# Performance work log

Hardware: AMD Instinct MI355X
Metric: run time of the kernel (lower is better)

The kernel has to match this reference:

```python
import jax, jax.numpy as jnp
import numpy as np

B, T, DIM, DZ = 512, 256, 128, 256
H = 2 * DZ  # LSTM hidden size (per direction)
RESIDUAL = False


def _lstm_cell(xt, h, c, Wih, Whh, bih, bhh):
    # PyTorch gate order: input, forget, cell, output
    g = xt @ Wih.T + bih + h @ Whh.T + bhh
    i, f, gg, o = jnp.split(g, 4, axis=-1)
    c2 = jax.nn.sigmoid(f) * c + jax.nn.sigmoid(i) * jnp.tanh(gg)
    h2 = jax.nn.sigmoid(o) * jnp.tanh(c2)
    return h2, c2


def _masked_lstm(xs, lengths, Wih, Whh, bih, bhh):
    # Packed-sequence semantics: state frozen and output zero past each length.
    Bn, Tn, _ = xs.shape
    Hn = Whh.shape[1]

    def step(carry, inp):
        h, c = carry
        xt, t = inp
        h2, c2 = _lstm_cell(xt, h, c, Wih, Whh, bih, bhh)
        m = (t < lengths)[:, None]
        h = jnp.where(m, h2, h)
        c = jnp.where(m, c2, c)
        return (h, c), jnp.where(m, h2, 0.0)

    init = (jnp.zeros((Bn, Hn), xs.dtype), jnp.zeros((Bn, Hn), xs.dtype))
    _, hs = jax.lax.scan(step, init, (xs.swapaxes(0, 1), jnp.arange(Tn)))
    return hs.swapaxes(0, 1)  # [B,T,H]


def setup_inputs() -> dict:
    key = jax.random.key(0)
    ks = jax.random.split(key, 24)
    rn = lambda k, *s: jax.random.normal(k, s, jnp.float32) * 0.02
    z = jnp.zeros
    return {
        "x": jax.random.normal(ks[0], (B, T, DIM), jnp.float32),
        "x_lengths": jax.random.randint(ks[1], (B,), 1, T + 1),
        "norm_g": jnp.ones((T, DIM)), "norm_b": z((T, DIM)),
        "We": rn(ks[2], DZ, DIM), "be": z((DZ,)),
        "Wih_f": rn(ks[3], 4 * H, DZ), "Whh_f": rn(ks[4], 4 * H, H),
        "bih_f": z((4 * H,)), "bhh_f": z((4 * H,)),
        "Wih_b": rn(ks[5], 4 * H, DZ), "Whh_b": rn(ks[6], 4 * H, H),
        "bih_b": z((4 * H,)), "bhh_b": z((4 * H,)),
        "W1e": rn(ks[7], H, 2 * H), "b1e": z((H,)),
        "W2e": rn(ks[8], DZ, H), "b2e": z((DZ,)),
        "Wd": rn(ks[9], DZ, DZ), "bd": z((DZ,)),
        "Wp1": rn(ks[10], DZ, DZ), "bp1": z((DZ,)),
        "Wp2": rn(ks[11], DIM, DZ), "bp2": z((DIM,)),
        "Wih_d": rn(ks[12], 4 * H, DZ + DIM), "Whh_d": rn(ks[13], 4 * H, H),
        "bih_d": z((4 * H,)), "bhh_d": z((4 * H,)),
        "W1d": rn(ks[14], DZ, H), "b1d": z((DZ,)),
        "W2d": rn(ks[15], DIM, DZ), "b2d": z((DIM,)),
    }


def _forward(x, x_lengths, norm_g, norm_b, We, be,
             Wih_f, Whh_f, bih_f, bhh_f, Wih_b, Whh_b, bih_b, bhh_b,
             W1e, b1e, W2e, b2e,
             Wd, bd, Wp1, bp1, Wp2, bp2,
             Wih_d, Whh_d, bih_d, bhh_d, W1d, b1d, W2d, b2d):
    # ----- encoder -----
    # LayerNorm over the last two dims [T, DIM] per sample
    mu = x.mean(axis=(1, 2), keepdims=True)
    var = x.var(axis=(1, 2), keepdims=True)
    xn = (x - mu) / jnp.sqrt(var + 1e-5) * norm_g + norm_b
    xe = jax.nn.relu(xn @ We.T + be)  # [B,T,DZ]

    hs_f = _masked_lstm(xe, x_lengths, Wih_f, Whh_f, bih_f, bhh_f)
    # backward direction: reverse each valid prefix, run, scatter back
    rev_idx = jnp.clip(x_lengths[:, None] - 1 - jnp.arange(T)[None, :], 0)  # [B,T]
    xe_rev = jnp.take_along_axis(xe, rev_idx[:, :, None], axis=1)
    hs_b_rev = _masked_lstm(xe_rev, x_lengths, Wih_b, Whh_b, bih_b, bhh_b)
    hs_b = jnp.take_along_axis(hs_b_rev, rev_idx[:, :, None], axis=1)
    valid = (jnp.arange(T)[None, :] < x_lengths[:, None])[:, :, None]
    out = jnp.concatenate([hs_f, jnp.where(valid, hs_b, 0.0)], axis=-1)  # [B,T,2H]
    out = out.sum(axis=1) / x_lengths[:, None].astype(x.dtype)
    out = jax.nn.relu(out @ W1e.T + b1e)
    zlat = out @ W2e.T + b2e  # [B,DZ]

    x0 = jax.nn.relu(zlat @ Wd.T + bd)
    pose0 = jax.nn.relu(x0 @ Wp1.T + bp1) @ Wp2.T + bp2  # [B,DIM]
    h0 = jnp.zeros((x.shape[0], H), x.dtype)

    def dstep(carry, _):
        h, c, pose = carry
        inp = jnp.concatenate([x0, pose], axis=1)
        h2, c2 = _lstm_cell(inp, h, c, Wih_d, Whh_d, bih_d, bhh_d)
        h_ = jax.nn.relu(h2 @ W1d.T + b1d)
        new_pose = h_ @ W2d.T + b2d
        if RESIDUAL:
            new_pose = new_pose + pose
        return (h2, c2, new_pose), new_pose

    _, poses = jax.lax.scan(dstep, (h0, h0, pose0), None, length=T)
    return poses.swapaxes(0, 1)  # [B,T,DIM]


def reference(x, x_lengths, norm_g, norm_b, We, be,
              Wih_f, Whh_f, bih_f, bhh_f, Wih_b, Whh_b, bih_b, bhh_b,
              W1e, b1e, W2e, b2e,
              Wd, bd, Wp1, bp1, Wp2, bp2,
              Wih_d, Whh_d, bih_d, bhh_d, W1d, b1d, W2d, b2d):
    dec = _forward(x, x_lengths, norm_g, norm_b, We, be,
                   Wih_f, Whh_f, bih_f, bhh_f, Wih_b, Whh_b, bih_b, bhh_b,
                   W1e, b1e, W2e, b2e,
                   Wd, bd, Wp1, bp1, Wp2, bp2,
                   Wih_d, Whh_d, bih_d, bhh_d, W1d, b1d, W2d, b2d)
    return (x, dec, x_lengths)
```

## Files before the change

kernel.cpp:

```cpp
#include <hip/hip_runtime.h>
#include <stdint.h>
#include <math.h>

typedef unsigned short u16;
typedef unsigned char u8;
typedef unsigned u32;
typedef unsigned long long u64;
typedef short s16x8 __attribute__((ext_vector_type(8)));
typedef int i32x2 __attribute__((ext_vector_type(2)));
typedef __bf16 bv8 __attribute__((ext_vector_type(8)));
typedef float f32x4 __attribute__((ext_vector_type(4)));

#define DEV static __device__ __forceinline__

DEV float b2f(u16 x){ union{unsigned u; float f;} v; v.u=((unsigned)x)<<16; return v.f; }
DEV u16 f2b(float f){ union{float f; unsigned u;} v; v.f=f; unsigned u=v.u; u += 0x7fff + ((u>>16)&1u); return (u16)(u>>16); }
DEV float sigm(float x){ return 1.f/(1.f+__expf(-x)); }
DEV float tanh_(float x){ float cx=fminf(fmaxf(x,-20.f),20.f); float e=__expf(2.f*cx); return (e-1.f)/(e+1.f); }
DEV f32x4 mfma16(bv8 a, bv8 b, f32x4 c){ return __builtin_amdgcn_mfma_f32_16x16x32_bf16(a,b,c,0,0,0); }
DEV f32x4 mfma8(u64 a, u64 b, f32x4 c){ return __builtin_amdgcn_mfma_f32_16x16x32_fp8_fp8((long)a,(long)b,c,0,0,0); }
DEV bv8 ldf(const u16* p){ return __builtin_bit_cast(bv8, *(const s16x8*)p); }
DEV bv8 cvt(const s16x8& v){ return __builtin_bit_cast(bv8, v); }
DEV u8 f2e4(float f){ return (u8)__builtin_amdgcn_cvt_pk_fp8_f32(f, f, 0, false); }

DEV unsigned ald4(const unsigned* p){ return __hip_atomic_load(p, __ATOMIC_RELAXED, __HIP_MEMORY_SCOPE_AGENT); }

DEV void gld16(s16x8& d, const u16* p){
  asm volatile("global_load_dwordx4 %0, %1, off sc0 sc1" : "=&v"(d) : "v"(p));
}
DEV void gld8(u64& d, const u8* p){
  asm volatile("global_load_dwordx2 %0, %1, off sc0 sc1" : "=&v"(d) : "v"(p));
}
DEV void gldc8(u64& d, const u8* p){
  asm volatile("global_load_dwordx2 %0, %1, off" : "=&v"(d) : "v"(p));
}
DEV void gst8(u16* p, u64 v){
  asm volatile("global_store_dwordx2 %0, %1, off sc0 sc1" :: "v"(p), "v"(v) : "memory");
}
DEV void gst4(u8* p, u32 v){
  asm volatile("global_store_dword %0, %1, off sc0 sc1" :: "v"(p), "v"(v) : "memory");
}
template<int N> DEV void wvm(){
  asm volatile("s_waitcnt vmcnt(%0)" :: "i"(N) : "memory");
  __builtin_amdgcn_sched_barrier(0);
}

DEV void arrive(unsigned* flags, int my, unsigned e){
  asm volatile("s_waitcnt vmcnt(0)" ::: "memory");
  __syncthreads();
  if (threadIdx.x==0)
    __hip_atomic_store(&flags[my*32], e, __ATOMIC_RELAXED, __HIP_MEMORY_SCOPE_AGENT);
}
DEV void waitflags(unsigned* flags, int lo, int n, unsigned e){
  int t = (int)threadIdx.x;
  if (t>=lo && t<lo+n){
    unsigned v;
    do {
      asm volatile("global_load_dword %0, %1, off sc0 sc1\ns_waitcnt vmcnt(0)" : "=&v"(v) : "v"(flags + t*32) : "memory");
      if (v>=e) break;
      __builtin_amdgcn_s_sleep(1);
    } while (1);
  }
  __syncthreads();
}

struct CvtJobs { const float* s[14]; u16* d[14]; int start[14]; };

__global__ __launch_bounds__(256) void cvt_w(CvtJobs J){
  int blk = blockIdx.x, tid = threadIdx.x;
  int j = 0;
  #pragma unroll
  for (int k=1;k<14;k++) if (blk >= J.start[k]) j = k;
  size_t idx = (size_t)(blk - J.start[j])*2048 + (size_t)tid*8;
  const f32x4* ps = (const f32x4*)(J.s[j] + idx);
  f32x4 a = ps[0], b = ps[1];
  s16x8 o;
  #pragma unroll
  for (int i=0;i<4;i++){ o[i]=(short)f2b(a[i]); o[4+i]=(short)f2b(b[i]); }
  *(s16x8*)(J.d[j] + idx) = o;
}

struct Cvt8Jobs { const float* s[4]; u8* d[4]; int start[4]; };

__global__ __launch_bounds__(256) void cvt_w8(Cvt8Jobs J){
  int blk = blockIdx.x, tid = threadIdx.x;
  int j = 0;
  #pragma unroll
  for (int k=1;k<4;k++) if (blk >= J.start[k]) j = k;
  size_t idx = (size_t)(blk - J.start[j])*2048 + (size_t)tid*8;
  const f32x4* ps = (const f32x4*)(J.s[j] + idx);
  f32x4 a = ps[0], b = ps[1];
  int w0 = __builtin_amdgcn_cvt_pk_fp8_f32(a[0]*64.f, a[1]*64.f, 0, false);
  w0 = __builtin_amdgcn_cvt_pk_fp8_f32(a[2]*64.f, a[3]*64.f, w0, true);
  int w1 = __builtin_amdgcn_cvt_pk_fp8_f32(b[0]*64.f, b[1]*64.f, 0, false);
  w1 = __builtin_amdgcn_cvt_pk_fp8_f32(b[2]*64.f, b[3]*64.f, w1, true);
  i32x2 o; o[0]=w0; o[1]=w1;
  *(i32x2*)(J.d[j] + idx) = o;
}

__global__ __launch_bounds__(256) void tr_w2d(const u16* __restrict__ in, u16* __restrict__ out){
  int idx = blockIdx.x*256 + threadIdx.x;
  int r = idx>>7, p = idx&127;
  out[idx] = in[p*256 + r];
}

__global__ __launch_bounds__(256) void pb_k(const float* __restrict__ Wihd, const float* __restrict__ b2d,
                                            float* __restrict__ pb){
  int g = blockIdx.x*256 + threadIdx.x;
  const float* row = Wihd + (size_t)g*384 + 256;
  float s = 0.f;
  for (int p=0;p<128;p++) s += row[p]*b2d[p];
  pb[g] = s;
}

__global__ __launch_bounds__(256) void ln_stats(const float* __restrict__ x,
                                                float* __restrict__ mu, float* __restrict__ rstd){
  int b = blockIdx.x;
  const float* xb = x + (size_t)b*32768;
  float s1=0.f, s2=0.f;
  for (int i = threadIdx.x*4; i < 32768; i += 256*4){
    f32x4 v = *(const f32x4*)(xb+i);
    #pragma unroll
    for (int j=0;j<4;j++){ float f = v[j]; s1+=f; s2+=f*f; }
  }
  #pragma unroll
  for (int o=32;o>0;o>>=1){ s1 += __shfl_down(s1,o); s2 += __shfl_down(s2,o); }
  __shared__ float r1[4], r2[4];
  int w = threadIdx.x>>6;
  if ((threadIdx.x&63)==0){ r1[w]=s1; r2[w]=s2; }
  __syncthreads();
  if (threadIdx.x==0){
    float a=0.f,c=0.f;
    for (int i=0;i<4;i++){ a+=r1[i]; c+=r2[i]; }
    float m=a/32768.f, v=c/32768.f-m*m;
    mu[b]=m; rstd[b]=1.f/sqrtf(v+1e-5f);
  }
}

__global__ __launch_bounds__(256) void ln_gemm(const float* __restrict__ x,
    const float* __restrict__ mu, const float* __restrict__ rstd,
    const float* __restrict__ g, const float* __restrict__ bn,
    const u16* __restrict__ Wb, const float* __restrict__ be, u8* __restrict__ xe){
  __shared__ __align__(16) u16 As[128*32];
  __shared__ __align__(16) u16 Ws[128*32];
  int tid=threadIdx.x, lane=tid&63, wid=tid>>6;
  int wr=wid>>1, wc=wid&1;
  long m0=(long)blockIdx.y*128, n0=(long)blockIdx.x*128;
  int lr=lane&15, lk=(lane>>4)*8;
  f32x4 acc[4][4];
  #pragma unroll
  for (int i=0;i<4;i++)
    #pragma unroll
    for (int j=0;j<4;j++) acc[i][j]=(f32x4){0.f,0.f,0.f,0.f};

  for (int k0=0;k0<128;k0+=32){
    __syncthreads();
    #pragma unroll
    for (int c=tid;c<512;c+=256){
      int row=c>>2, kb=(c&3)*8;
      long R=m0+row;
      int b=(int)(R>>8), tt=(int)(R&255);
      float m=mu[b], rs=rstd[b];
      const f32x4* px=(const f32x4*)(x + R*128 + k0+kb);
      const f32x4* pg=(const f32x4*)(g + tt*128 + k0+kb);
      const f32x4* pb=(const f32x4*)(bn + tt*128 + k0+kb);
      f32x4 x0=px[0], x1=px[1], g0=pg[0], g1=pg[1], b0=pb[0], b1=pb[1];
      s16x8 o;
      #pragma unroll
      for (int j=0;j<4;j++){
        o[j]   = (short)f2b((x0[j]-m)*rs*g0[j] + b0[j]);
        o[4+j] = (short)f2b((x1[j]-m)*rs*g1[j] + b1[j]);
      }
      *(s16x8*)(As + row*32 + kb) = o;
    }
    #pragma unroll
    for (int c=tid;c<512;c+=256){
      int row=c>>2, kb=(c&3)*8;
      *(s16x8*)(Ws + row*32 + kb) = *(const s16x8*)(Wb + (n0+row)*128 + k0+kb);
    }
    __syncthreads();
    bv8 af[4], bf[4];
    #pragma unroll
    for (int i=0;i<4;i++) af[i] = ldf(As + (wr*64+i*16+lr)*32 + lk);
    #pragma unroll
    for (int j=0;j<4;j++) bf[j] = ldf(Ws + (wc*64+j*16+lr)*32 + lk);
    #pragma unroll
    for (int i=0;i<4;i++)
      #pragma unroll
      for (int j=0;j<4;j++) acc[i][j] = mfma16(af[i], bf[j], acc[i][j]);
  }
  #pragma unroll
  for (int i=0;i<4;i++)
    #pragma unroll
    for (int j=0;j<4;j++)
      #pragma unroll
      for (int r=0;r<4;r++){
        int m = wr*64+i*16+(lane>>4)*4+r;
        int n = wc*64+j*16+lr;
        float v = acc[i][j][r] + be[n0+n];
        xe[(m0+m)*256 + n0+n] = f2e4(fmaxf(v,0.f)*16.f);
      }
}

template<int BM, int BN, bool RELU, bool OUTF32>
__global__ __launch_bounds__(256) void gemm_bt(const u16* __restrict__ A, int lda,
                                               const u16* __restrict__ W, int ldw,
                                               const float* __restrict__ bias1, const float* __restrict__ bias2,
                                               u16* __restrict__ Cb, float* __restrict__ Cf, int ldc, int K){
  constexpr int BK=32;
  constexpr int FM=BM/32, FN=BN/32;
  __shared__ __align__(16) u16 As[BM*BK];
  __shared__ __align__(16) u16 Ws[BN*BK];
  int tid=threadIdx.x, lane=tid&63, wid=tid>>6;
  int wr=wid>>1, wc=wid&1;
  long m0=(long)blockIdx.y*BM, n0=(long)blockIdx.x*BN;
  int lr=lane&15, lk=(lane>>4)*8;
  f32x4 acc[FM][FN];
  #pragma unroll
  for (int i=0;i<FM;i++)
    #pragma unroll
    for (int j=0;j<FN;j++) acc[i][j] = (f32x4){0.f,0.f,0.f,0.f};
  for (int k0=0;k0<K;k0+=BK){
    __syncthreads();
    #pragma unroll
    for (int c=tid;c<BM*4;c+=256){
      int row=c>>2, kb=(c&3)*8;
      *(s16x8*)(As + row*BK + kb) = *(const s16x8*)(A + (m0+row)*lda + k0+kb);
    }
    #pragma unroll
    for (int c=tid;c<BN*4;c+=256){
      int row=c>>2, kb=(c&3)*8;
      *(s16x8*)(Ws + row*BK + kb) = *(const s16x8*)(W + (n0+row)*ldw + k0+kb);
    }
    __syncthreads();
    bv8 af[FM], bf[FN];
    #pragma unroll
    for (int i=0;i<FM;i++) af[i] = ldf(As + (wr*(BM/2)+i*16+lr)*BK + lk);
    #pragma unroll
    for (int j=0;j<FN;j++) bf[j] = ldf(Ws + (wc*(BN/2)+j*16+lr)*BK + lk);
    #pragma unroll
    for (int i=0;i<FM;i++)
      #pragma unroll
      for (int j=0;j<FN;j++) acc[i][j] = mfma16(af[i], bf[j], acc[i][j]);
  }
  #pragma unroll
  for (int i=0;i<FM;i++)
    #pragma unroll
    for (int j=0;j<FN;j++)
      #pragma unroll
      for (int r=0;r<4;r++){
        int m = wr*(BM/2)+i*16+(lane>>4)*4+r;
        int n = wc*(BN/2)+j*16+lr;
        float v = acc[i][j][r];
        if (bias1) v += bias1[n0+n];
        if (bias2) v += bias2[n0+n];
        if (RELU) v = fmaxf(v,0.f);
        if (OUTF32) Cf[(m0+m)*ldc + n0+n] = v;
        else        Cb[(m0+m)*ldc + n0+n] = f2b(v);
      }
}

struct EncP {
  const u8* xe; const int* lens;
  const u8 *Wihf8,*Whhf8,*Wihb8,*Whhb8;
  const float *bif,*bhf,*bib,*bhb;
  u8 *hf0,*hf1,*hb0,*hb1;
  u16* pooled;
  unsigned* flags;
};

__global__ __launch_bounds__(512,1) void enc_persist(EncP P){
  __shared__ __align__(16) u8 Wl[64*776];
  __shared__ __align__(4)  u8 Hs[128*16];
  const int tid=threadIdx.x, lane=tid&63, w=tid>>6;
  const int bx=blockIdx.x;
  const int grp=bx&7, kc=bx>>3;
  const int dir=grp>>2, bt=grp&3;
  const int lr=lane&15, q8=(lane>>4)*8;
  unsigned* flags = P.flags + grp*2048;
  const u8* Wih8 = dir? P.Wihb8 : P.Wihf8;
  const u8* Whh8 = dir? P.Whhb8 : P.Whhf8;
  const float* bi = dir? P.bib : P.bif;
  const float* bh = dir? P.bhb : P.bhf;
  u8* h0 = dir? P.hb0 : P.hf0;
  u8* h1 = dir? P.hb1 : P.hf1;

  for (int idx=tid; idx<64*96; idx+=512){
    int row=idx/96, col8=(idx%96)*8;
    int g=row>>4, c=row&15;
    size_t grow=(size_t)(g*512 + kc*16 + c);
    const u8* src = (col8<256)? (Wih8 + grow*256 + col8) : (Whh8 + grow*512 + (col8-256));
    *(u64*)(Wl + (size_t)row*776 + col8) = *(const u64*)src;
  }
  const int cg = kc*16 + lr;
  const float b_i=bi[cg]+bh[cg], b_f=bi[512+cg]+bh[512+cg];
  const float b_g=bi[1024+cg]+bh[1024+cg], b_o=bi[1536+cg]+bh[1536+cg];
  const float gsc = 1.f/1024.f;
  const int r0 = w*16 + lr;
  const int slen0 = P.lens[bt*128+r0];
  const u8* xb0 = P.xe + (size_t)(bt*128+r0)*256;
  int elen[4]; float cs[4], hh[4], asum[4];
  #pragma unroll
  for (int r=0;r<4;r++){
    int m=w*16+(lane>>4)*4+r;
    elen[r]=P.lens[bt*128+m];
    cs[r]=0.f; hh[r]=0.f; asum[r]=0.f;
  }
  __syncthreads();

  u64 rx[8];
  auto issue_rx=[&](int t_){
    int tt = dir? max(slen0-1-t_,0) : t_;
    const u8* xr = xb0 + (size_t)tt*256;
    #pragma unroll
    for (int j=0;j<8;j++) gldc8(rx[j], xr + j*32 + q8);
  };
  issue_rx(0);

  for (int t=0;t<256;t++){
    const u8* hp = (t&1)? h1 : h0;
    u8*       hn = (t&1)? h0 : h1;
    waitflags(flags, 0, 32, (unsigned)t);
    u64 fb[16];
    {
      const u8* hr = hp + (size_t)(bt*128+r0)*512;
      #pragma unroll
      for (int j=0;j<16;j++) gld8(fb[j], hr + j*32 + q8);
    }
    wvm<16>();
    f32x4 acc[4];
    #pragma unroll
    for (int g=0;g<4;g++) acc[g]=(f32x4){0.f,0.f,0.f,0.f};
    #pragma unroll
    for (int j=0;j<8;j++){
      u64 a = rx[j];
      #pragma unroll
      for (int g=0;g<4;g++){
        u64 b = *(const u64*)(Wl + (size_t)(g*16+lr)*776 + j*32 + q8);
        acc[g]=mfma8(a,b,acc[g]);
      }
    }
    wvm<8>();
    #pragma unroll
    for (int j=0;j<8;j++){
      u64 a = fb[j];
      #pragma unroll
      for (int g=0;g<4;g++){
        u64 b = *(const u64*)(Wl + (size_t)(g*16+lr)*776 + 256 + j*32 + q8);
        acc[g]=mfma8(a,b,acc[g]);
      }
    }
    wvm<0>();
    #pragma unroll
    for (int j=8;j<16;j++){
      u64 a = fb[j];
      #pragma unroll
      for (int g=0;g<4;g++){
        u64 b = *(const u64*)(Wl + (size_t)(g*16+lr)*776 + 256 + j*32 + q8);
        acc[g]=mfma8(a,b,acc[g]);
      }
    }
    #pragma unroll
    for (int r=0;r<4;r++){
      int m=w*16+(lane>>4)*4+r;
      if (t<elen[r]){
        float iv=sigm(acc[0][r]*gsc+b_i), fv=sigm(acc[1][r]*gsc+b_f);
        float gv=tanh_(acc[2][r]*gsc+b_g), ov=sigm(acc[3][r]*gsc+b_o);
        float c2=fv*cs[r]+iv*gv, h2v=ov*tanh_(c2);
        cs[r]=c2; hh[r]=h2v; asum[r]+=h2v;
      }
      Hs[m*16+lr]=f2e4(hh[r]*16.f);
    }
    __syncthreads();
    {
      int sm=tid>>2, pt=tid&3;
      gst4(hn + (size_t)(bt*128+sm)*512 + kc*16 + pt*4, *(const u32*)(Hs + sm*16 + pt*4));
    }
    arrive(flags, kc, (unsigned)(t+1));
    if (t<255) issue_rx(t+1);
  }
  #pragma unroll
  for (int r=0;r<4;r++){
    int m=w*16+(lane>>4)*4+r;
    P.pooled[(size_t)(bt*128+m)*1024 + (size_t)dir*512 + cg]=f2b(asum[r]/(float)elen[r]);
  }
}

struct DecP {
  const u16 *Whhd, *Wcmp, *W1d, *W2d;
  const float *gix, *gp0, *pb, *b1d, *b2d;
  u16 *h0,*h1,*r1a,*r1b;
  float* outd;
  unsigned* flags;
};

__global__ __launch_bounds__(256,1) void dec_persist(DecP P){
  __shared__ __align__(16) u16 Wh [64*520];
  __shared__ __align__(16) u16 WcL[64*264];
  __shared__ __align__(16) u16 F12[16*520];
  __shared__ __align__(16) u16 Hs[64*16];
  const int tid=threadIdx.x, lane=tid&63, w=tid>>6;
  const int bx=blockIdx.x;
  const int grp=bx&7, kc=bx>>3;
  const int g0 = grp*64;
  const int lr=lane&15, lk=(lane>>4)*8;
  unsigned* flags = P.flags + grp*2048;

  for (int idx=tid; idx<64*64; idx+=256){
    int row=idx>>6, col=(idx&63)*8;
    int g=row>>4, c=row&15;
    size_t grow=(size_t)(g*512+kc*16+c);
    *(s16x8*)(Wh + row*520 + col) = *(const s16x8*)(P.Whhd + grow*512 + col);
  }
  for (int idx=tid; idx<64*32; idx+=256){
    int row=idx>>5, col=(idx&31)*8;
    int g=row>>4, c=row&15;
    size_t grow=(size_t)(g*512+kc*16+c);
    *(s16x8*)(WcL + row*264 + col) = *(const s16x8*)(P.Wcmp + grow*256 + col);
  }
  if (kc<16){
    for (int idx=tid; idx<16*64; idx+=256){
      int rr=idx>>6, col=(idx&63)*8;
      *(s16x8*)(F12 + rr*520 + col) = *(const s16x8*)(P.W1d + (size_t)(kc*16+rr)*512 + col);
    }
  } else if (kc<24){
    for (int idx=tid; idx<16*32; idx+=256){
      int rr=idx>>5, col=(idx&31)*8;
      *(s16x8*)(F12 + rr*264 + col) = *(const s16x8*)(P.W2d + (size_t)((kc-16)*16+rr)*256 + col);
    }
  }
  float gx[4][4]; float pbr[4];
  #pragma unroll
  for (int g=0;g<4;g++)
    #pragma unroll
    for (int r=0;r<4;r++){
      int m=w*16+(lane>>4)*4+r;
      gx[g][r]=P.gix[(size_t)(g0+m)*2048 + (size_t)g*512 + kc*16 + lr];
    }
  #pragma unroll
  for (int g=0;g<4;g++) pbr[g] = P.pb[(size_t)g*512 + kc*16 + lr];
  const float b1=(kc<16)? P.b1d[kc*16+lr] : 0.f;
  const float b2=(kc>=16&&kc<24)? P.b2d[(kc-16)*16+lr] : 0.f;
  const int ar = w*16 + lr;
  float cs[4];
  f32x4 gh[4];
  #pragma unroll
  for (int r=0;r<4;r++) cs[r]=0.f;
  #pragma unroll
  for (int g=0;g<4;g++) gh[g]=(f32x4){0.f,0.f,0.f,0.f};
  __syncthreads();

  for (int t=0;t<256;t++){
    const u16* r1rd = (t&1)? P.r1b : P.r1a;
    u16* hn = (t&1)? P.h0 : P.h1;
    f32x4 acc[4];
    if (t==0){
      #pragma unroll
      for (int g=0;g<4;g++)
        #pragma unroll
        for (int r=0;r<4;r++){
          int m=w*16+(lane>>4)*4+r;
          acc[g][r] = gx[g][r] + P.gp0[(size_t)(g0+m)*2048 + (size_t)g*512 + kc*16 + lr];
        }
    } else {
      waitflags(flags, 32, 16, (unsigned)t);
      #pragma unroll
      for (int g=0;g<4;g++){
        acc[g] = (f32x4){gx[g][0]+pbr[g], gx[g][1]+pbr[g], gx[g][2]+pbr[g], gx[g][3]+pbr[g]};
        acc[g] = acc[g] + gh[g];
      }
      const u16* rb = r1rd + (size_t)(g0+ar)*256;
      s16x8 fb[8];
      #pragma unroll
      for (int k=0;k<4;k++){
        gld16(fb[k*2],   rb + k*64 + lk);
        gld16(fb[k*2+1], rb + k*64 + 32 + lk);
      }
      wvm<0>();
      #pragma unroll
      for (int k=0;k<4;k++)
        #pragma unroll
        for (int kk=0;kk<2;kk++){
          bv8 a=cvt(fb[k*2+kk]);
          #pragma unroll
          for (int g=0;g<4;g++){
            bv8 bf=ldf(WcL + (g*16+lr)*264 + k*64 + kk*32 + lk);
            acc[g]=mfma16(a,bf,acc[g]);
          }
        }
    }
    #pragma unroll
    for (int r=0;r<4;r++){
      float iv=sigm(acc[0][r]), fv=sigm(acc[1][r]);
      float gv=tanh_(acc[2][r]), ov=sigm(acc[3][r]);
      float c2=fv*cs[r]+iv*gv, h2v=ov*tanh_(c2);
      cs[r]=c2;
      int m=w*16+(lane>>4)*4+r;
      Hs[m*16+lr]=f2b(h2v);
    }
    __syncthreads();
    {
      int sm=tid>>2, pt=tid&3;
      gst8(hn + (size_t)(g0+sm)*512 + kc*16 + pt*4, *(const u64*)(Hs + sm*16 + pt*4));
    }
    arrive(flags, kc, (unsigned)(t+1));
    if (kc>=16 && kc<24 && t>0){
      const u16* rb = r1rd + (size_t)(g0+ar)*256;
      f32x4 fa2=(f32x4){0.f,0.f,0.f,0.f};
      s16x8 fb[8];
      #pragma unroll
      for (int k=0;k<4;k++){
        gld16(fb[k*2],   rb + k*64 + lk);
        gld16(fb[k*2+1], rb + k*64 + 32 + lk);
      }
      wvm<0>();
      #pragma unroll
      for (int k=0;k<4;k++)
        #pragma unroll
        for (int kk=0;kk<2;kk++){
          bv8 a=cvt(fb[k*2+kk]);
          bv8 bf=ldf(F12 + lr*264 + k*64 + kk*32 + lk);
          fa2=mfma16(a,bf,fa2);
        }
      int pc=(kc-16)*16+lr;
      #pragma unroll
      for (int r=0;r<4;r++){
        int m=w*16+(lane>>4)*4+r;
        __builtin_nontemporal_store(fa2[r]+b2, P.outd + (size_t)(g0+m)*32768 + (size_t)(t-1)*128 + pc);
      }
    }
    waitflags(flags, 0, 32, (unsigned)(t+1));
    f32x4 gn[4]; f32x4 fa=(f32x4){0.f,0.f,0.f,0.f};
    #pragma unroll
    for (int g=0;g<4;g++) gn[g]=(f32x4){0.f,0.f,0.f,0.f};
    {
      const u16* hb = hn + (size_t)(g0+ar)*512;
      s16x8 fb[2][8];
      auto issue=[&](int b, int h4){
        const u16* p = hb + h4*256;
        #pragma unroll
        for (int k=0;k<4;k++){
          gld16(fb[b][k*2],   p + k*64 + lk);
          gld16(fb[b][k*2+1], p + k*64 + 32 + lk);
        }
      };
      issue(0,0); issue(1,1);
      #pragma unroll
      for (int h4=0;h4<2;h4++){
        if (h4==0) wvm<8>(); else wvm<0>();
        #pragma unroll
        for (int k=0;k<4;k++)
          #pragma unroll
          for (int kk=0;kk<2;kk++){
            bv8 a=cvt(fb[h4][k*2+kk]);
            int col = h4*256 + k*64 + kk*32;
            #pragma unroll
            for (int g=0;g<4;g++){
              bv8 bf=ldf(Wh + (g*16+lr)*520 + col + lk);
              gn[g]=mfma16(a,bf,gn[g]);
            }
            if (kc<16){
              bv8 bf=ldf(F12 + lr*520 + col + lk);
              fa=mfma16(a,bf,fa);
            }
          }
      }
    }
    #pragma unroll
    for (int g=0;g<4;g++) gh[g]=gn[g];
    if (kc<16){
      u16* r1w = (t&1)? P.r1a : P.r1b;
      #pragma unroll
      for (int r=0;r<4;r++){
        int m=w*16+(lane>>4)*4+r;
        Hs[m*16+lr]=f2b(fmaxf(fa[r]+b1,0.f));
      }
      __syncthreads();
      {
        int sm=tid>>2, pt=tid&3;
        gst8(r1w + (size_t)(g0+sm)*256 + kc*16 + pt*4, *(const u64*)(Hs + sm*16 + pt*4));
      }
      arrive(flags, 32+kc, (unsigned)(t+1));
    }
  }
  if (kc>=16 && kc<24){
    waitflags(flags, 32, 16, 256u);
    const u16* rb = P.r1a + (size_t)(g0+ar)*256;
    f32x4 fa2=(f32x4){0.f,0.f,0.f,0.f};
    s16x8 fb[8];
    #pragma unroll
    for (int k=0;k<4;k++){
      gld16(fb[k*2],   rb + k*64 + lk);
      gld16(fb[k*2+1], rb + k*64 + 32 + lk);
    }
    wvm<0>();
    #pragma unroll
    for (int k=0;k<4;k++)
      #pragma unroll
      for (int kk=0;kk<2;kk++){
        bv8 a=cvt(fb[k*2+kk]);
        bv8 bf=ldf(F12 + lr*264 + k*64 + kk*32 + lk);
        fa2=mfma16(a,bf,fa2);
      }
    int pc=(kc-16)*16+lr;
    #pragma unroll
    for (int r=0;r<4;r++){
      int m=w*16+(lane>>4)*4+r;
      __builtin_nontemporal_store(fa2[r]+b2, P.outd + (size_t)(g0+m)*32768 + (size_t)255*128 + pc);
    }
  }
}

__global__ __launch_bounds__(512) void len_cast(const int* __restrict__ lens, float* __restrict__ out){
  int i = threadIdx.x;
  if (i < 512) out[i] = (float)lens[i];
}

extern "C" void kernel_launch(void* const* d_in, const int* in_sizes, int n_in,
                              void* d_out, int out_size, void* d_ws, size_t ws_size,
                              hipStream_t stream){
  (void)in_sizes; (void)n_in; (void)out_size; (void)ws_size;
  const float* x      = (const float*)d_in[0];
  const int*   lens   = (const int*)d_in[1];
  const float* ng     = (const float*)d_in[2];
  const float* nb     = (const float*)d_in[3];
  const float* We     = (const float*)d_in[4];
  const float* be     = (const float*)d_in[5];
  const float* Wih_f  = (const float*)d_in[6];
  const float* Whh_f  = (const float*)d_in[7];
  const float* bih_f  = (const float*)d_in[8];
  const float* bhh_f  = (const float*)d_in[9];
  const float* Wih_b  = (const float*)d_in[10];
  const float* Whh_b  = (const float*)d_in[11];
  const float* bih_b  = (const float*)d_in[12];
  const float* bhh_b  = (const float*)d_in[13];
  const float* W1e    = (const float*)d_in[14];
  const float* b1e    = (const float*)d_in[15];
  const float* W2e    = (const float*)d_in[16];
  const float* b2e    = (const float*)d_in[17];
  const float* Wd     = (const float*)d_in[18];
  const float* bd     = (const float*)d_in[19];
  const float* Wp1    = (const float*)d_in[20];
  const float* bp1    = (const float*)d_in[21];
  const float* Wp2    = (const float*)d_in[22];
  const float* bp2    = (const float*)d_in[23];
  const float* Wih_d  = (const float*)d_in[24];
  const float* Whh_d  = (const float*)d_in[25];
  const float* bih_d  = (const float*)d_in[26];
  const float* bhh_d  = (const float*)d_in[27];
  const float* W1d    = (const float*)d_in[28];
  const float* b1d    = (const float*)d_in[29];
  const float* W2d    = (const float*)d_in[30];
  const float* b2d    = (const float*)d_in[31];

  char* p = (char*)d_ws;
  auto carve = [&](size_t bytes)->void*{ void* r=(void*)p; p += (bytes+255)&~(size_t)255; return r; };
  float* mu   = (float*)carve(512*4);
  float* rstd = (float*)carve(512*4);
  u8* xe8     = (u8*)carve((size_t)33554432);
  u16* wWe  = (u16*)carve(32768*2);
  u16* wIhf = (u16*)carve(524288*2);
  u16* wHhf = (u16*)carve(1048576*2);
  u16* wIhb = (u16*)carve(524288*2);
  u16* wHhb = (u16*)carve(1048576*2);
  u16* wW1e = (u16*)carve(524288*2);
  u16* wW2e = (u16*)carve(131072*2);
  u16* wWd  = (u16*)carve(65536*2);
  u16* wWp1 = (u16*)carve(65536*2);
  u16* wWp2 = (u16*)carve(32768*2);
  u16* wIhd = (u16*)carve(786432*2);
  u16* wHhd = (u16*)carve(1048576*2);
  u16* wW1d = (u16*)carve(131072*2);
  u16* wW2d = (u16*)carve(32768*2);
  u16* wW2dT  = (u16*)carve(32768*2);
  u16* wWcomp = (u16*)carve(524288*2);
  u8* wIhf8 = (u8*)carve(524288);
  u8* wHhf8 = (u8*)carve(1048576);
  u8* wIhb8 = (u8*)carve(524288);
  u8* wHhb8 = (u8*)carve(1048576);
  float* pbv  = (float*)carve(2048*4);
  float* gp0f = (float*)carve((size_t)1048576*4);
  u8* hf0  = (u8*)carve(262144);
  u8* hf1  = (u8*)carve(262144);
  u8* hb0  = (u8*)carve(262144);
  u8* hb1  = (u8*)carve(262144);
  u16* hd0  = (u16*)carve(524288);
  u16* hd1  = (u16*)carve(524288);
  u16* r1a  = (u16*)carve(262144);
  u16* r1b  = (u16*)carve(262144);
  u16* pooled = (u16*)carve(1048576);
  u16* out1   = (u16*)carve(524288);
  u16* zlat   = (u16*)carve(262144);
  u16* x0     = (u16*)carve(262144);
  u16* t0     = (u16*)carve(262144);
  float* gix  = (float*)carve(4194304);
  u16* pose   = (u16*)carve(131072);
  unsigned* barflags = (unsigned*)carve(16*2048*4);

  float* out_x   = (float*)d_out;
  float* out_dec = out_x + 16777216;
  float* out_len = out_x + 33554432;

  hipMemcpyAsync(out_x, x, (size_t)16777216*4, hipMemcpyDeviceToDevice, stream);
  hipMemsetAsync(hf0,0,262144,stream);
  hipMemsetAsync(hb0,0,262144,stream);
  hipMemsetAsync(barflags,0,16*2048*4,stream);

  CvtJobs J;
  const float* srcs[14] = {We,Wih_f,Whh_f,Wih_b,Whh_b,W1e,W2e,Wd,Wp1,Wp2,Wih_d,Whh_d,W1d,W2d};
  u16* dsts[14] = {wWe,wIhf,wHhf,wIhb,wHhb,wW1e,wW2e,wWd,wWp1,wWp2,wIhd,wHhd,wW1d,wW2d};
  int ns[14] = {32768,524288,1048576,524288,1048576,524288,131072,65536,65536,32768,786432,1048576,131072,32768};
  int blk=0;
  for (int i=0;i<14;i++){ J.s[i]=srcs[i]; J.d[i]=dsts[i]; J.start[i]=blk; blk += ns[i]/2048; }
  cvt_w<<<blk,256,0,stream>>>(J);

  Cvt8Jobs J8;
  const float* s8[4] = {Wih_f,Whh_f,Wih_b,Whh_b};
  u8* d8[4] = {wIhf8,wHhf8,wIhb8,wHhb8};
  int n8[4] = {524288,1048576,524288,1048576};
  int blk8=0;
  for (int i=0;i<4;i++){ J8.s[i]=s8[i]; J8.d[i]=d8[i]; J8.start[i]=blk8; blk8 += n8[i]/2048; }
  cvt_w8<<<blk8,256,0,stream>>>(J8);

  tr_w2d<<<128,256,0,stream>>>(wW2d, wW2dT);
  pb_k<<<8,256,0,stream>>>(Wih_d, b2d, pbv);
  gemm_bt<64,64,false,false><<<dim3(4,32),256,0,stream>>>(wIhd+256,384, wW2dT,128, nullptr,nullptr, wWcomp,nullptr,256,128);

  ln_stats<<<512,256,0,stream>>>(x,mu,rstd);
  ln_gemm<<<dim3(2,1024),256,0,stream>>>(x,mu,rstd,ng,nb,wWe,be,xe8);

  EncP EP = {xe8,lens,wIhf8,wHhf8,wIhb8,wHhb8,bih_f,bhh_f,bih_b,bhh_b,hf0,hf1,hb0,hb1,pooled,barflags};
  {
    void* ea[] = {&EP};
    if (hipLaunchCooperativeKernel((void*)enc_persist, dim3(256), dim3(512), ea, 0, stream) != hipSuccess)
      enc_persist<<<256,512,0,stream>>>(EP);
  }

  gemm_bt<64,64,true ,false><<<dim3(8,8),256,0,stream>>>(pooled,1024,wW1e,1024,b1e,nullptr,out1,nullptr,512,1024);
  gemm_bt<64,64,false,false><<<dim3(4,8),256,0,stream>>>(out1,512,wW2e,512,b2e,nullptr,zlat,nullptr,256,512);
  gemm_bt<64,64,true ,false><<<dim3(4,8),256,0,stream>>>(zlat,256,wWd,256,bd,nullptr,x0,nullptr,256,256);
  gemm_bt<64,64,true ,false><<<dim3(4,8),256,0,stream>>>(x0,256,wWp1,256,bp1,nullptr,t0,nullptr,256,256);
  gemm_bt<64,64,false,false><<<dim3(2,8),256,0,stream>>>(t0,256,wWp2,256,bp2,nullptr,pose,nullptr,128,256);
  gemm_bt<64,128,false,true><<<dim3(16,8),256,0,stream>>>(x0,256,wIhd,384,bih_d,bhh_d,nullptr,gix,2048,256);
  gemm_bt<64,128,false,true><<<dim3(16,8),256,0,stream>>>(pose,128,wIhd+256,384,nullptr,nullptr,nullptr,gp0f,2048,128);

  DecP DP = {wHhd,wWcomp,wW1d,wW2d, gix,gp0f,pbv,b1d,b2d, hd0,hd1,r1a,r1b, out_dec, barflags + 8*2048};
  {
    void* da[] = {&DP};
    if (hipLaunchCooperativeKernel((void*)dec_persist, dim3(256), dim3(256), da, 0, stream) != hipSuccess)
      dec_persist<<<256,256,0,stream>>>(DP);
  }

  len_cast<<<1,512,0,stream>>>(lens,out_len);
}
```

Baseline: 3.980 ms.

## Move decoder persistent LSTM to FP8 weights and states with split flag waits

Converts the decoder recurrent weights (Whh_d, W1d, W2d, composed Wcomp) and the exchanged hidden/relu state buffers from bf16 to scaled FP8, and switches decoder MFMAs to the fp8 16x16x32 variant with rescaling by 1/1024. This halves global traffic for the per-step state exchange and shared-memory footprint. It also splits the flag waits in both encoder and decoder into two halves so loads for the first half of K start before all producers have arrived. The cost is reduced numerical precision in the decoder recurrence, which may drift from the reference over 256 steps.

```diff
diff --git a/kernel.cpp b/kernel.cpp
--- a/kernel.cpp
+++ b/kernel.cpp
@@ -20,22 +20,15 @@
 DEV f32x4 mfma16(bv8 a, bv8 b, f32x4 c){ return __builtin_amdgcn_mfma_f32_16x16x32_bf16(a,b,c,0,0,0); }
 DEV f32x4 mfma8(u64 a, u64 b, f32x4 c){ return __builtin_amdgcn_mfma_f32_16x16x32_fp8_fp8((long)a,(long)b,c,0,0,0); }
 DEV bv8 ldf(const u16* p){ return __builtin_bit_cast(bv8, *(const s16x8*)p); }
-DEV bv8 cvt(const s16x8& v){ return __builtin_bit_cast(bv8, v); }
 DEV u8 f2e4(float f){ return (u8)__builtin_amdgcn_cvt_pk_fp8_f32(f, f, 0, false); }
 
 DEV unsigned ald4(const unsigned* p){ return __hip_atomic_load(p, __ATOMIC_RELAXED, __HIP_MEMORY_SCOPE_AGENT); }
 
-DEV void gld16(s16x8& d, const u16* p){
-  asm volatile("global_load_dwordx4 %0, %1, off sc0 sc1" : "=&v"(d) : "v"(p));
-}
 DEV void gld8(u64& d, const u8* p){
   asm volatile("global_load_dwordx2 %0, %1, off sc0 sc1" : "=&v"(d) : "v"(p));
 }
 DEV void gldc8(u64& d, const u8* p){
   asm volatile("global_load_dwordx2 %0, %1, off" : "=&v"(d) : "v"(p));
-}
-DEV void gst8(u16* p, u64 v){
-  asm volatile("global_store_dwordx2 %0, %1, off sc0 sc1" :: "v"(p), "v"(v) : "memory");
 }
 DEV void gst4(u8* p, u32 v){
   asm volatile("global_store_dword %0, %1, off sc0 sc1" :: "v"(p), "v"(v) : "memory");
@@ -80,13 +73,13 @@
   *(s16x8*)(J.d[j] + idx) = o;
 }
 
-struct Cvt8Jobs { const float* s[4]; u8* d[4]; int start[4]; };
+struct Cvt8Jobs { const float* s[7]; u8* d[7]; int start[7]; };
 
 __global__ __launch_bounds__(256) void cvt_w8(Cvt8Jobs J){
   int blk = blockIdx.x, tid = threadIdx.x;
   int j = 0;
   #pragma unroll
-  for (int k=1;k<4;k++) if (blk >= J.start[k]) j = k;
+  for (int k=1;k<7;k++) if (blk >= J.start[k]) j = k;
   size_t idx = (size_t)(blk - J.start[j])*2048 + (size_t)tid*8;
   const f32x4* ps = (const f32x4*)(J.s[j] + idx);
   f32x4 a = ps[0], b = ps[1];
@@ -96,6 +89,17 @@
   w1 = __builtin_amdgcn_cvt_pk_fp8_f32(b[2]*64.f, b[3]*64.f, w1, true);
   i32x2 o; o[0]=w0; o[1]=w1;
   *(i32x2*)(J.d[j] + idx) = o;
+}
+
+__global__ __launch_bounds__(256) void cvt_b8(const u16* __restrict__ in, u8* __restrict__ out){
+  int idx = (blockIdx.x*256 + threadIdx.x)*8;
+  s16x8 v = *(const s16x8*)(in+idx);
+  int w0 = __builtin_amdgcn_cvt_pk_fp8_f32(b2f((u16)v[0])*64.f, b2f((u16)v[1])*64.f, 0, false);
+  w0 = __builtin_amdgcn_cvt_pk_fp8_f32(b2f((u16)v[2])*64.f, b2f((u16)v[3])*64.f, w0, true);
+  int w1 = __builtin_amdgcn_cvt_pk_fp8_f32(b2f((u16)v[4])*64.f, b2f((u16)v[5])*64.f, 0, false);
+  w1 = __builtin_amdgcn_cvt_pk_fp8_f32(b2f((u16)v[6])*64.f, b2f((u16)v[7])*64.f, w1, true);
+  i32x2 o; o[0]=w0; o[1]=w1;
+  *(i32x2*)(out + idx) = o;
 }
 
 __global__ __launch_bounds__(256) void tr_w2d(const u16* __restrict__ in, u16* __restrict__ out){
@@ -320,17 +324,18 @@
   for (int t=0;t<256;t++){
     const u8* hp = (t&1)? h1 : h0;
     u8*       hn = (t&1)? h0 : h1;
-    waitflags(flags, 0, 32, (unsigned)t);
     u64 fb[16];
-    {
-      const u8* hr = hp + (size_t)(bt*128+r0)*512;
-      #pragma unroll
-      for (int j=0;j<16;j++) gld8(fb[j], hr + j*32 + q8);
-    }
+    const u8* hr = hp + (size_t)(bt*128+r0)*512;
+    waitflags(flags, 0, 16, (unsigned)t);
+    #pragma unroll
+    for (int j=0;j<8;j++) gld8(fb[j], hr + j*32 + q8);
+    waitflags(flags, 16, 16, (unsigned)t);
+    #pragma unroll
+    for (int j=8;j<16;j++) gld8(fb[j], hr + j*32 + q8);
+    f32x4 acc[4];
+    #pragma unroll
+    for (int g=0;g<4;g++) acc[g]=(f32x4){0.f,0.f,0.f,0.f};
     wvm<16>();
-    f32x4 acc[4];
-    #pragma unroll
-    for (int g=0;g<4;g++) acc[g]=(f32x4){0.f,0.f,0.f,0.f};
     #pragma unroll
     for (int j=0;j<8;j++){
       u64 a = rx[j];
@@ -387,46 +392,46 @@
 }
 
 struct DecP {
-  const u16 *Whhd, *Wcmp, *W1d, *W2d;
+  const u8 *Whhd8, *Wcmp8, *W1d8, *W2d8;
   const float *gix, *gp0, *pb, *b1d, *b2d;
-  u16 *h0,*h1,*r1a,*r1b;
+  u8 *h0,*h1,*r1a,*r1b;
   float* outd;
   unsigned* flags;
 };
 
 __global__ __launch_bounds__(256,1) void dec_persist(DecP P){
-  __shared__ __align__(16) u16 Wh [64*520];
-  __shared__ __align__(16) u16 WcL[64*264];
-  __shared__ __align__(16) u16 F12[16*520];
-  __shared__ __align__(16) u16 Hs[64*16];
+  __shared__ __align__(8) u8 Wh [64*520];
+  __shared__ __align__(8) u8 Wc [64*264];
+  __shared__ __align__(8) u8 F12[16*520];
+  __shared__ __align__(4) u8 Hs[64*16];
   const int tid=threadIdx.x, lane=tid&63, w=tid>>6;
   const int bx=blockIdx.x;
   const int grp=bx&7, kc=bx>>3;
   const int g0 = grp*64;
-  const int lr=lane&15, lk=(lane>>4)*8;
+  const int lr=lane&15, q8=(lane>>4)*8;
   unsigned* flags = P.flags + grp*2048;
 
   for (int idx=tid; idx<64*64; idx+=256){
-    int row=idx>>6, col=(idx&63)*8;
+    int row=idx>>6, col8=(idx&63)*8;
     int g=row>>4, c=row&15;
     size_t grow=(size_t)(g*512+kc*16+c);
-    *(s16x8*)(Wh + row*520 + col) = *(const s16x8*)(P.Whhd + grow*512 + col);
+    *(u64*)(Wh + (size_t)row*520 + col8) = *(const u64*)(P.Whhd8 + grow*512 + col8);
   }
   for (int idx=tid; idx<64*32; idx+=256){
-    int row=idx>>5, col=(idx&31)*8;
+    int row=idx>>5, col8=(idx&31)*8;
     int g=row>>4, c=row&15;
     size_t grow=(size_t)(g*512+kc*16+c);
-    *(s16x8*)(WcL + row*264 + col) = *(const s16x8*)(P.Wcmp + grow*256 + col);
+    *(u64*)(Wc + (size_t)row*264 + col8) = *(const u64*)(P.Wcmp8 + grow*256 + col8);
   }
   if (kc<16){
     for (int idx=tid; idx<16*64; idx+=256){
-      int rr=idx>>6, col=(idx&63)*8;
-      *(s16x8*)(F12 + rr*520 + col) = *(const s16x8*)(P.W1d + (size_t)(kc*16+rr)*512 + col);
+      int rr=idx>>6, col8=(idx&63)*8;
+      *(u64*)(F12 + (size_t)rr*520 + col8) = *(const u64*)(P.W1d8 + (size_t)(kc*16+rr)*512 + col8);
     }
   } else if (kc<24){
     for (int idx=tid; idx<16*32; idx+=256){
-      int rr=idx>>5, col=(idx&31)*8;
-      *(s16x8*)(F12 + rr*264 + col) = *(const s16x8*)(P.W2d + (size_t)((kc-16)*16+rr)*256 + col);
+      int rr=idx>>5, col8=(idx&31)*8;
+      *(u64*)(F12 + (size_t)rr*264 + col8) = *(const u64*)(P.W2d8 + (size_t)((kc-16)*16+rr)*256 + col8);
     }
   }
   float gx[4][4]; float pbr[4];
@@ -441,6 +446,7 @@
   for (int g=0;g<4;g++) pbr[g] = P.pb[(size_t)g*512 + kc*16 + lr];
   const float b1=(kc<16)? P.b1d[kc*16+lr] : 0.f;
   const float b2=(kc>=16&&kc<24)? P.b2d[(kc-16)*16+lr] : 0.f;
+  const float gsc = 1.f/1024.f;
   const int ar = w*16 + lr;
   float cs[4];
   f32x4 gh[4];
@@ -451,10 +457,11 @@
   __syncthreads();
 
   for (int t=0;t<256;t++){
-    const u16* r1rd = (t&1)? P.r1b : P.r1a;
-    u16* hn = (t&1)? P.h0 : P.h1;
-    f32x4 acc[4];
+    const u8* r1rd = (t&1)? P.r1b : P.r1a;
+    u8* hn = (t&1)? P.h0 : P.h1;
+    f32x4 acc[4]; float ascale;
     if (t==0){
+      ascale = 1.f;
       #pragma unroll
       for (int g=0;g<4;g++)
         #pragma unroll
@@ -463,150 +470,148 @@
           acc[g][r] = gx[g][r] + P.gp0[(size_t)(g0+m)*2048 + (size_t)g*512 + kc*16 + lr];
         }
     } else {
-      waitflags(flags, 32, 16, (unsigned)t);
-      #pragma unroll
-      for (int g=0;g<4;g++){
-        acc[g] = (f32x4){gx[g][0]+pbr[g], gx[g][1]+pbr[g], gx[g][2]+pbr[g], gx[g][3]+pbr[g]};
-        acc[g] = acc[g] + gh[g];
-      }
-      const u16* rb = r1rd + (size_t)(g0+ar)*256;
-      s16x8 fb[8];
-      #pragma unroll
-      for (int k=0;k<4;k++){
-        gld16(fb[k*2],   rb + k*64 + lk);
-        gld16(fb[k*2+1], rb + k*64 + 32 + lk);
+      ascale = gsc;
+      const u8* rb = r1rd + (size_t)(g0+ar)*256;
+      u64 fb[8];
+      waitflags(flags, 32, 8, (unsigned)t);
+      #pragma unroll
+      for (int j=0;j<4;j++) gld8(fb[j], rb + j*32 + q8);
+      waitflags(flags, 40, 8, (unsigned)t);
+      #pragma unroll
+      for (int j=4;j<8;j++) gld8(fb[j], rb + j*32 + q8);
+      #pragma unroll
+      for (int g=0;g<4;g++)
+        acc[g] = gh[g] + (f32x4){(gx[g][0]+pbr[g])*1024.f,(gx[g][1]+pbr[g])*1024.f,
+                                 (gx[g][2]+pbr[g])*1024.f,(gx[g][3]+pbr[g])*1024.f};
+      wvm<4>();
+      #pragma unroll
+      for (int j=0;j<4;j++){
+        u64 a=fb[j];
+        #pragma unroll
+        for (int g=0;g<4;g++){
+          u64 b = *(const u64*)(Wc + (size_t)(g*16+lr)*264 + j*32 + q8);
+          acc[g]=mfma8(a,b,acc[g]);
+        }
       }
       wvm<0>();
       #pragma unroll
-      for (int k=0;k<4;k++)
+      for (int j=4;j<8;j++){
+        u64 a=fb[j];
         #pragma unroll
-        for (int kk=0;kk<2;kk++){
-          bv8 a=cvt(fb[k*2+kk]);
-          #pragma unroll
-          for (int g=0;g<4;g++){
-            bv8 bf=ldf(WcL + (g*16+lr)*264 + k*64 + kk*32 + lk);
-            acc[g]=mfma16(a,bf,acc[g]);
-          }
+        for (int g=0;g<4;g++){
+          u64 b = *(const u64*)(Wc + (size_t)(g*16+lr)*264 + j*32 + q8);
+          acc[g]=mfma8(a,b,acc[g]);
         }
+      }
     }
     #pragma unroll
     for (int r=0;r<4;r++){
-      float iv=sigm(acc[0][r]), fv=sigm(acc[1][r]);
-      float gv=tanh_(acc[2][r]), ov=sigm(acc[3][r]);
+      float iv=sigm(acc[0][r]*ascale), fv=sigm(acc[1][r]*ascale);
+      float gv=tanh_(acc[2][r]*ascale), ov=sigm(acc[3][r]*ascale);
       float c2=fv*cs[r]+iv*gv, h2v=ov*tanh_(c2);
       cs[r]=c2;
       int m=w*16+(lane>>4)*4+r;
-      Hs[m*16+lr]=f2b(h2v);
+      Hs[m*16+lr]=f2e4(h2v*16.f);
     }
     __syncthreads();
     {
       int sm=tid>>2, pt=tid&3;
-      gst8(hn + (size_t)(g0+sm)*512 + kc*16 + pt*4, *(const u64*)(Hs + sm*16 + pt*4));
+      gst4(hn + (size_t)(g0+sm)*512 + kc*16 + pt*4, *(const u32*)(Hs + sm*16 + pt*4));
     }
     arrive(flags, kc, (unsigned)(t+1));
     if (kc>=16 && kc<24 && t>0){
-      const u16* rb = r1rd + (size_t)(g0+ar)*256;
+      const u8* rb = r1rd + (size_t)(g0+ar)*256;
       f32x4 fa2=(f32x4){0.f,0.f,0.f,0.f};
-      s16x8 fb[8];
-      #pragma unroll
-      for (int k=0;k<4;k++){
-        gld16(fb[k*2],   rb + k*64 + lk);
-        gld16(fb[k*2+1], rb + k*64 + 32 + lk);
-      }
+      u64 fb[8];
+      #pragma unroll
+      for (int j=0;j<8;j++) gld8(fb[j], rb + j*32 + q8);
       wvm<0>();
       #pragma unroll
-      for (int k=0;k<4;k++)
-        #pragma unroll
-        for (int kk=0;kk<2;kk++){
-          bv8 a=cvt(fb[k*2+kk]);
-          bv8 bf=ldf(F12 + lr*264 + k*64 + kk*32 + lk);
-          fa2=mfma16(a,bf,fa2);
-        }
+      for (int j=0;j<8;j++){
+        u64 b = *(const u64*)(F12 + (size_t)lr*264 + j*32 + q8);
+        fa2=mfma8(fb[j],b,fa2);
+      }
       int pc=(kc-16)*16+lr;
       #pragma unroll
       for (int r=0;r<4;r++){
         int m=w*16+(lane>>4)*4+r;
-        __builtin_nontemporal_store(fa2[r]+b2, P.outd + (size_t)(g0+m)*32768 + (size_t)(t-1)*128 + pc);
-      }
-    }
-    waitflags(flags, 0, 32, (unsigned)(t+1));
+        __builtin_nontemporal_store(fa2[r]*gsc+b2, P.outd + (size_t)(g0+m)*32768 + (size_t)(t-1)*128 + pc);
+      }
+    }
+    u64 hbf[16];
+    const u8* hb = hn + (size_t)(g0+ar)*512;
+    waitflags(flags, 0, 16, (unsigned)(t+1));
+    #pragma unroll
+    for (int j=0;j<8;j++) gld8(hbf[j], hb + j*32 + q8);
+    waitflags(flags, 16, 16, (unsigned)(t+1));
+    #pragma unroll
+    for (int j=8;j<16;j++) gld8(hbf[j], hb + j*32 + q8);
     f32x4 gn[4]; f32x4 fa=(f32x4){0.f,0.f,0.f,0.f};
     #pragma unroll
     for (int g=0;g<4;g++) gn[g]=(f32x4){0.f,0.f,0.f,0.f};
-    {
-      const u16* hb = hn + (size_t)(g0+ar)*512;
-      s16x8 fb[2][8];
-      auto issue=[&](int b, int h4){
-        const u16* p = hb + h4*256;
-        #pragma unroll
-        for (int k=0;k<4;k++){
-          gld16(fb[b][k*2],   p + k*64 + lk);
-          gld16(fb[b][k*2+1], p + k*64 + 32 + lk);
-        }
-      };
-      issue(0,0); issue(1,1);
-      #pragma unroll
-      for (int h4=0;h4<2;h4++){
-        if (h4==0) wvm<8>(); else wvm<0>();
-        #pragma unroll
-        for (int k=0;k<4;k++)
-          #pragma unroll
-          for (int kk=0;kk<2;kk++){
-            bv8 a=cvt(fb[h4][k*2+kk]);
-            int col = h4*256 + k*64 + kk*32;
-            #pragma unroll
-            for (int g=0;g<4;g++){
-              bv8 bf=ldf(Wh + (g*16+lr)*520 + col + lk);
-              gn[g]=mfma16(a,bf,gn[g]);
-            }
-            if (kc<16){
-              bv8 bf=ldf(F12 + lr*520 + col + lk);
-              fa=mfma16(a,bf,fa);
-            }
-          }
+    wvm<8>();
+    #pragma unroll
+    for (int j=0;j<8;j++){
+      u64 a=hbf[j];
+      #pragma unroll
+      for (int g=0;g<4;g++){
+        u64 b = *(const u64*)(Wh + (size_t)(g*16+lr)*520 + j*32 + q8);
+        gn[g]=mfma8(a,b,gn[g]);
+      }
+      if (kc<16){
+        u64 b = *(const u64*)(F12 + (size_t)lr*520 + j*32 + q8);
+        fa=mfma8(a,b,fa);
+      }
+    }
+    wvm<0>();
+    #pragma unroll
+    for (int j=8;j<16;j++){
+      u64 a=hbf[j];
+      #pragma unroll
+      for (int g=0;g<4;g++){
+        u64 b = *(const u64*)(Wh + (size_t)(g*16+lr)*520 + j*32 + q8);
+        gn[g]=mfma8(a,b,gn[g]);
+      }
+      if (kc<16){
+        u64 b = *(const u64*)(F12 + (size_t)lr*520 + j*32 + q8);
+        fa=mfma8(a,b,fa);
       }
     }
     #pragma unroll
     for (int g=0;g<4;g++) gh[g]=gn[g];
     if (kc<16){
-      u16* r1w = (t&1)? P.r1a : P.r1b;
+      u8* r1w = (t&1)? P.r1a : P.r1b;
       #pragma unroll
       for (int r=0;r<4;r++){
         int m=w*16+(lane>>4)*4+r;
-        Hs[m*16+lr]=f2b(fmaxf(fa[r]+b1,0.f));
+        Hs[m*16+lr]=f2e4(fmaxf(fa[r]*gsc+b1,0.f)*16.f);
       }
       __syncthreads();
       {
         int sm=tid>>2, pt=tid&3;
-        gst8(r1w + (size_t)(g0+sm)*256 + kc*16 + pt*4, *(const u64*)(Hs + sm*16 + pt*4));
+        gst4(r1w + (size_t)(g0+sm)*256 + kc*16 + pt*4, *(const u32*)(Hs + sm*16 + pt*4));
       }
       arrive(flags, 32+kc, (unsigned)(t+1));
     }
   }
   if (kc>=16 && kc<24){
     waitflags(flags, 32, 16, 256u);
-    const u16* rb = P.r1a + (size_t)(g0+ar)*256;
+    const u8* rb = P.r1a + (size_t)(g0+ar)*256;
     f32x4 fa2=(f32x4){0.f,0.f,0.f,0.f};
-    s16x8 fb[8];
-    #pragma unroll
-    for (int k=0;k<4;k++){
-      gld16(fb[k*2],   rb + k*64 + lk);
-      gld16(fb[k*2+1], rb + k*64 + 32 + lk);
-    }
+    u64 fb[8];
+    #pragma unroll
+    for (int j=0;j<8;j++) gld8(fb[j], rb + j*32 + q8);
     wvm<0>();
     #pragma unroll
-    for (int k=0;k<4;k++)
-      #pragma unroll
-      for (int kk=0;kk<2;kk++){
-        bv8 a=cvt(fb[k*2+kk]);
-        bv8 bf=ldf(F12 + lr*264 + k*64 + kk*32 + lk);
-        fa2=mfma16(a,bf,fa2);
-      }
+    for (int j=0;j<8;j++){
+      u64 b = *(const u64*)(F12 + (size_t)lr*264 + j*32 + q8);
+      fa2=mfma8(fb[j],b,fa2);
+    }
     int pc=(kc-16)*16+lr;
     #pragma unroll
     for (int r=0;r<4;r++){
       int m=w*16+(lane>>4)*4+r;
-      __builtin_nontemporal_store(fa2[r]+b2, P.outd + (size_t)(g0+m)*32768 + (size_t)255*128 + pc);
+      __builtin_nontemporal_store(fa2[r]*gsc+b2, P.outd + (size_t)(g0+m)*32768 + (size_t)255*128 + pc);
     }
   }
 }
@@ -678,16 +683,20 @@
   u8* wHhf8 = (u8*)carve(1048576);
   u8* wIhb8 = (u8*)carve(524288);
   u8* wHhb8 = (u8*)carve(1048576);
+  u8* wHhd8 = (u8*)carve(1048576);
+  u8* wW1d8 = (u8*)carve(131072);
+  u8* wW2d8 = (u8*)carve(32768);
+  u8* wWcmp8= (u8*)carve(524288);
   float* pbv  = (float*)carve(2048*4);
   float* gp0f = (float*)carve((size_t)1048576*4);
   u8* hf0  = (u8*)carve(262144);
   u8* hf1  = (u8*)carve(262144);
   u8* hb0  = (u8*)carve(262144);
   u8* hb1  = (u8*)carve(262144);
-  u16* hd0  = (u16*)carve(524288);
-  u16* hd1  = (u16*)carve(524288);
-  u16* r1a  = (u16*)carve(262144);
-  u16* r1b  = (u16*)carve(262144);
+  u8* hd0  = (u8*)carve(262144);
+  u8* hd1  = (u8*)carve(262144);
+  u8* r1a8 = (u8*)carve(131072);
+  u8* r1b8 = (u8*)carve(131072);
   u16* pooled = (u16*)carve(1048576);
   u16* out1   = (u16*)carve(524288);
   u16* zlat   = (u16*)carve(262144);
@@ -704,6 +713,7 @@
   hipMemcpyAsync(out_x, x, (size_t)16777216*4, hipMemcpyDeviceToDevice, stream);
   hipMemsetAsync(hf0,0,262144,stream);
   hipMemsetAsync(hb0,0,262144,stream);
+  hipMemsetAsync(hd0,0,262144,stream);
   hipMemsetAsync(barflags,0,16*2048*4,stream);
 
   CvtJobs J;
@@ -715,16 +725,17 @@
   cvt_w<<<blk,256,0,stream>>>(J);
 
   Cvt8Jobs J8;
-  const float* s8[4] = {Wih_f,Whh_f,Wih_b,Whh_b};
-  u8* d8[4] = {wIhf8,wHhf8,wIhb8,wHhb8};
-  int n8[4] = {524288,1048576,524288,1048576};
+  const float* s8[7] = {Wih_f,Whh_f,Wih_b,Whh_b,Whh_d,W1d,W2d};
+  u8* d8[7] = {wIhf8,wHhf8,wIhb8,wHhb8,wHhd8,wW1d8,wW2d8};
+  int n8[7] = {524288,1048576,524288,1048576,1048576,131072,32768};
   int blk8=0;
-  for (int i=0;i<4;i++){ J8.s[i]=s8[i]; J8.d[i]=d8[i]; J8.start[i]=blk8; blk8 += n8[i]/2048; }
+  for (int i=0;i<7;i++){ J8.s[i]=s8[i]; J8.d[i]=d8[i]; J8.start[i]=blk8; blk8 += n8[i]/2048; }
   cvt_w8<<<blk8,256,0,stream>>>(J8);
 
   tr_w2d<<<128,256,0,stream>>>(wW2d, wW2dT);
   pb_k<<<8,256,0,stream>>>(Wih_d, b2d, pbv);
   gemm_bt<64,64,false,false><<<dim3(4,32),256,0,stream>>>(wIhd+256,384, wW2dT,128, nullptr,nullptr, wWcomp,nullptr,256,128);
+  cvt_b8<<<256,256,0,stream>>>(wWcomp, wWcmp8);
 
   ln_stats<<<512,256,0,stream>>>(x,mu,rstd);
   ln_gemm<<<dim3(2,1024),256,0,stream>>>(x,mu,rstd,ng,nb,wWe,be,xe8);
@@ -744,7 +755,7 @@
   gemm_bt<64,128,false,true><<<dim3(16,8),256,0,stream>>>(x0,256,wIhd,384,bih_d,bhh_d,nullptr,gix,2048,256);
   gemm_bt<64,128,false,true><<<dim3(16,8),256,0,stream>>>(pose,128,wIhd+256,384,nullptr,nullptr,nullptr,gp0f,2048,128);
 
-  DecP DP = {wHhd,wWcomp,wW1d,wW2d, gix,gp0f,pbv,b1d,b2d, hd0,hd1,r1a,r1b, out_dec, barflags + 8*2048};
+  DecP DP = {wHhd8,wWcmp8,wW1d8,wW2d8, gix,gp0f,pbv,b1d,b2d, hd0,hd1,r1a8,r1b8, out_dec, barflags + 8*2048};
   {
     void* da[] = {&DP};
     if (hipLaunchCooperativeKernel((void*)dec_persist, dim3(256), dim3(256), da, 0, stream) != hipSuccess)
```

New measurement: 4.088 ms. 1.03x slower.
